# Optimization experiments

Measured on AMD Instinct MI355X. Metric: run time of the kernel, lower is better.

Reference implementation:

```python
import jax, jax.numpy as jnp
import numpy as np

H = 64        # HIDDEN_DIM
V = 64        # VOCAB_SIZE
INNER = 16    # INNER_DIM
LR = 0.01     # INFERENCE_LR
B = 256
L = 2048
EPS = 1e-5    # LayerNorm eps (torch default)


def setup_inputs() -> dict:
    key = jax.random.key(0)
    ks = jax.random.split(key, 8)

    def lin(k, fi, fo):
        return jax.random.normal(k, (fi, fo), jnp.float32) / np.sqrt(fi).astype(np.float32)

    return {
        "seq": jax.random.randint(ks[0], (B, L), 0, V),
        "embed": jax.random.normal(ks[1], (V, H), jnp.float32) * 0.02,
        "ff_w1": lin(ks[2], H, 2 * H), "ff_b1": jnp.zeros((2 * H,), jnp.float32),
        "ff_w2": lin(ks[3], 2 * H, H), "ff_b2": jnp.zeros((H,), jnp.float32),
        "ln_g": jnp.ones((H,), jnp.float32), "ln_b": jnp.zeros((H,), jnp.float32),
        "w1": lin(ks[4], H, INNER), "b1": jnp.zeros((INNER,), jnp.float32),
        "w2": lin(ks[5], INNER, H), "b2": jnp.zeros((H,), jnp.float32),
        "out_w": lin(ks[6], H, V), "out_b": jnp.zeros((V,), jnp.float32),
    }


def _mlp(p, x):
    W1, B1, W2, B2 = p
    return jnp.maximum(x @ W1 + B1, 0.0) @ W2 + B2


def reference(seq, embed, ff_w1, ff_b1, ff_w2, ff_b2, ln_g, ln_b,
              w1, b1, w2, b2, out_w, out_b):
    # Encoder: embed -> residual FFN -> LayerNorm
    e = embed[seq]                                        # [B,L,H]
    ff = jnp.maximum(e @ ff_w1 + ff_b1, 0.0) @ ff_w2 + ff_b2
    h = e + ff
    mu = h.mean(-1, keepdims=True)
    var = ((h - mu) ** 2).mean(-1, keepdims=True)
    hs = (h - mu) / jnp.sqrt(var + EPS) * ln_g + ln_b     # [B,L,H]
    hs = jax.lax.stop_gradient(hs)                        # all TTT inputs are .detach()ed in torch

    T = (L - 2) // 2                                      # len(range(0, L-3, 2))
    idx = jnp.arange(T) * 2
    k_seq = hs[:, idx]                                    # [B,T,H]
    v_seq = hs[:, idx + 1]                                # [B,T,H]

    # base params copied via load_state_dict -> no grad connection
    p0 = tuple(jax.lax.stop_gradient(p) for p in (w1, b1, w2, b2))

    def ttt(kseq, vseq, qlast):
        def step(p, kv):
            k, v = kv
            g = jax.grad(lambda pp: jnp.mean((_mlp(pp, k) - v) ** 2))(p)
            return jax.tree_util.tree_map(lambda a, ga: a - LR * ga, p, g), None
        pf, _ = jax.lax.scan(step, p0, (kseq, vseq))
        return _mlp(pf, qlast)                            # [H]

    ctx = jax.vmap(ttt)(k_seq, v_seq, hs[:, -1])          # [B,H]
    ctx = jax.lax.stop_gradient(ctx)                      # torch builds ctx under no_grad
    return ctx @ out_w + out_b                            # [B,V]
```

## Files before the change

kernel.cpp:

```cpp
#include <hip/hip_runtime.h>

#define TSTEPS 1023
#define GAMMA  (0.01f / 32.0f)
#define EPSV   1e-5f

#define WS_HS 0
#define WS_G  4096
#define WS_Z0 8192

typedef float v2f __attribute__((ext_vector_type(2)));
typedef unsigned int v2u __attribute__((ext_vector_type(2)));

template<int CTRL>
__device__ __forceinline__ float dppmov(float x) {
    return __int_as_float(__builtin_amdgcn_update_dpp(0, __float_as_int(x), CTRL, 0xF, 0xF, true));
}
__device__ __forceinline__ v2u swap16(float a, float b) {
    return __builtin_amdgcn_permlane16_swap(__float_as_uint(a), __float_as_uint(b), false, false);
}
__device__ __forceinline__ v2u swap32(float a, float b) {
    return __builtin_amdgcn_permlane32_swap(__float_as_uint(a), __float_as_uint(b), false, false);
}
__device__ __forceinline__ float rlane(float v, int sl) {
    return __int_as_float(__builtin_amdgcn_readlane(__float_as_int(v), sl));
}
#define U2F(x) __uint_as_float(x)

__global__ void hs_kernel(const float* __restrict__ embed,
                          const float* __restrict__ ffw1, const float* __restrict__ ffb1,
                          const float* __restrict__ ffw2, const float* __restrict__ ffb2,
                          const float* __restrict__ lng,  const float* __restrict__ lnb,
                          float* __restrict__ ws) {
    __shared__ float e[64];
    __shared__ float a1[128];
    int w = blockIdx.x;
    int tid = threadIdx.x;
    if (tid < 64) e[tid] = embed[w * 64 + tid];
    __syncthreads();
    float z1 = ffb1[tid];
    for (int x = 0; x < 64; ++x) z1 += e[x] * ffw1[x * 128 + tid];
    a1[tid] = fmaxf(z1, 0.0f);
    __syncthreads();
    if (tid < 64) {
        float f = ffb2[tid];
        for (int i = 0; i < 128; ++i) f += a1[i] * ffw2[i * 64 + tid];
        float hv = e[tid] + f;
        float s = hv;
#pragma unroll
        for (int m = 32; m >= 1; m >>= 1) s += __shfl_xor(s, m);
        float mu = s * (1.0f / 64.0f);
        float dv = hv - mu;
        float vs = dv * dv;
#pragma unroll
        for (int m = 32; m >= 1; m >>= 1) vs += __shfl_xor(vs, m);
        float rstd = 1.0f / sqrtf(vs * (1.0f / 64.0f) + EPSV);
        ws[WS_HS + w * 64 + tid] = dv * rstd * lng[tid] + lnb[tid];
    }
}

__global__ void gz_kernel(const float* __restrict__ w1, const float* __restrict__ b1,
                          float* __restrict__ ws) {
    __shared__ float row[64];
    int w = blockIdx.x, tid = threadIdx.x;
    row[tid] = ws[WS_HS + w * 64 + tid];
    __syncthreads();
    float g = 0.0f;
    for (int x = 0; x < 64; ++x) g += row[x] * ws[WS_HS + tid * 64 + x];
    ws[WS_G + w * 64 + tid] = GAMMA * g + GAMMA;
    if (tid < 16) {
        float z = b1[tid];
        for (int x = 0; x < 64; ++x) z += row[x] * w1[x * 16 + tid];
        ws[WS_Z0 + w * 16 + tid] = z;
    }
}

struct TTT4Smem {
    float hs[4096];
    float Gs[4096];
    int   sq[2048];
    float ybuf[2][4][64];
    float ctxp[4][64];
};

__device__ __forceinline__ void reduce4(const v2f* a2, const v2f* p2, v2f* dz2) {
    float q0 = p2[0].x + dppmov<0xB1>(p2[1].x);
    float q1 = p2[0].y + dppmov<0xB1>(p2[1].y);
    float rm0 = (a2[0].x > 0.0f) ? q0 : 0.0f;
    float rm1 = (a2[0].y > 0.0f) ? q1 : 0.0f;
    v2u f01 = swap16(rm0, rm1);
    float T = U2F(f01[0]) + U2F(f01[1]);
    v2u g01 = swap32(T, T);
    T = U2F(g01[0]) + U2F(g01[1]);
    T = T + dppmov<0x122>(T);
    T = T + dppmov<0x124>(T);
    T = T + dppmov<0x128>(T);
    v2u u01 = swap16(T, T);
    const float A0 = U2F(u01[0]);
    const float A1 = U2F(u01[1]);
    dz2[0] = {A0, A1};
    dz2[1] = {dppmov<0xB1>(A0), dppmov<0xB1>(A1)};
}

__launch_bounds__(256, 1)
__global__ void ttt_kernel(const int* __restrict__ seq,
                           const float* __restrict__ w2, const float* __restrict__ b2i,
                           const float* __restrict__ outw, const float* __restrict__ outb,
                           const float* __restrict__ ws, float* __restrict__ out) {
    __shared__ TTT4Smem sm;

    const int b    = blockIdx.x;
    const int tid  = threadIdx.x;
    const int wv   = tid >> 6;
    const int lane = tid & 63;
    const int b0   = lane & 1;
    const int X    = b0 << 1;
    const bool pb  = (b0 != 0);
    const bool wv0 = (wv == 0);

    {
        float4*       hv = (float4*)sm.hs;
        const float4* sv = (const float4*)(ws + WS_HS);
#pragma unroll
        for (int m = 0; m < 4; ++m) hv[m * 256 + tid] = sv[m * 256 + tid];
        float4*       gv = (float4*)sm.Gs;
        const float4* gs = (const float4*)(ws + WS_G);
#pragma unroll
        for (int m = 0; m < 4; ++m) gv[m * 256 + tid] = gs[m * 256 + tid];
        int4*       qv = (int4*)sm.sq;
        const int4* qs = (const int4*)(seq + b * 2048);
#pragma unroll
        for (int m = 0; m < 2; ++m) qv[m * 256 + tid] = qs[m * 256 + tid];
    }

    v2f Zv[2];
    {
        const float4 z0 = *(const float4*)(ws + WS_Z0 + lane * 16 + 4 * wv);
        Zv[0] = {z0.x, z0.y};
        Zv[1] = {z0.z, z0.w};
    }

    v2f W2p[2];
#pragma unroll
    for (int i = 0; i < 2; ++i) {
        v2f w;
        w.x = w2[(4 * wv + ((2 * i) ^ X)) * 64 + lane];
        w.y = w2[(4 * wv + ((2 * i + 1) ^ X)) * 64 + lane];
        W2p[i] = w;
    }
    float ybias = wv0 ? b2i[lane] : 0.0f;
    const float gma = wv0 ? GAMMA : 0.0f;
    __syncthreads();

    int tk = sm.sq[0];
    v2f z2[2];
    {
        const int stk = __builtin_amdgcn_readfirstlane(tk);
        const float e0 = rlane(Zv[0].x, stk);
        const float e1 = rlane(Zv[0].y, stk);
        const float e2 = rlane(Zv[1].x, stk);
        const float e3 = rlane(Zv[1].y, stk);
        z2[0] = { pb ? e2 : e0, pb ? e3 : e1 };
        z2[1] = { pb ? e0 : e2, pb ? e1 : e3 };
    }
    float vv = sm.hs[sm.sq[1] * 64 + lane];

    int2 pairT  = *(const int2*)(sm.sq + 2);
    int2 pairT1 = *(const int2*)(sm.sq + 4);

#pragma unroll 2
    for (int t = 0; t < TSTEPS - 1; ++t) {
        const int tkn = pairT.x;
        const int tvn = pairT.y;
        const int par = t & 1;

        const v2f zero2 = {0.0f, 0.0f};
        v2f a2[2];
        a2[0] = __builtin_elementwise_max(z2[0], zero2);
        a2[1] = __builtin_elementwise_max(z2[1], zero2);
        v2f accv = a2[0] * W2p[0] + a2[1] * W2p[1];
        const float ypart = ybias + accv.x + accv.y;

        sm.ybuf[par][wv][lane] = ypart;
        __syncthreads();
        const float y0 = sm.ybuf[par][0][lane];
        const float y1 = sm.ybuf[par][1][lane];
        const float y2 = sm.ybuf[par][2][lane];
        const float y3 = sm.ybuf[par][3][lane];

        const float vnext = sm.hs[tvn * 64 + lane];
        const float cr = sm.Gs[tk * 64 + lane];
        const int2 pairT2 = *(const int2*)(sm.sq + 2 * t + 6);
        const int stkn = __builtin_amdgcn_readfirstlane(tkn);
        const float e0 = rlane(Zv[0].x, stkn);
        const float e1 = rlane(Zv[0].y, stkn);
        const float e2 = rlane(Zv[1].x, stkn);
        const float e3 = rlane(Zv[1].y, stkn);
        const v2f E0 = { pb ? e2 : e0, pb ? e3 : e1 };
        const v2f E1 = { pb ? e0 : e2, pb ? e1 : e3 };
        const float cz = rlane(cr, stkn);

        const float d = ((y0 + y1) + (y2 + y3)) - vv;

        const v2f d2 = {d, d};
        v2f p2[2];
        p2[0] = W2p[0] * d2;
        p2[1] = W2p[1] * d2;
        const float sd = GAMMA * d;
        ybias -= gma * d;
        const v2f sd2 = {sd, sd};
        W2p[0] = W2p[0] - sd2 * a2[0];
        W2p[1] = W2p[1] - sd2 * a2[1];

        v2f dz2[2];
        reduce4(a2, p2, dz2);

        const v2f cz2 = {cz, cz};
        z2[0] = E0 - cz2 * dz2[0];
        z2[1] = E1 - cz2 * dz2[1];

        const v2f dzl0 = pb ? dz2[1] : dz2[0];
        const v2f dzl1 = pb ? dz2[0] : dz2[1];
        const v2f cr2 = {cr, cr};
        Zv[0] = Zv[0] - cr2 * dzl0;
        Zv[1] = Zv[1] - cr2 * dzl1;

        vv = vnext;
        tk = tkn;
        pairT = pairT1;
        pairT1 = pairT2;
    }

    {
        const int tkn = pairT.y;
        const v2f zero2 = {0.0f, 0.0f};
        v2f a2[2];
        a2[0] = __builtin_elementwise_max(z2[0], zero2);
        a2[1] = __builtin_elementwise_max(z2[1], zero2);
        v2f accv = a2[0] * W2p[0] + a2[1] * W2p[1];
        const float ypart = ybias + accv.x + accv.y;

        sm.ybuf[0][wv][lane] = ypart;
        __syncthreads();
        const float y0 = sm.ybuf[0][0][lane];
        const float y1 = sm.ybuf[0][1][lane];
        const float y2 = sm.ybuf[0][2][lane];
        const float y3 = sm.ybuf[0][3][lane];

        const float cr = sm.Gs[tk * 64 + lane];
        const int stkn = __builtin_amdgcn_readfirstlane(tkn);
        const float e0 = rlane(Zv[0].x, stkn);
        const float e1 = rlane(Zv[0].y, stkn);
        const float e2 = rlane(Zv[1].x, stkn);
        const float e3 = rlane(Zv[1].y, stkn);
        const v2f E0 = { pb ? e2 : e0, pb ? e3 : e1 };
        const v2f E1 = { pb ? e0 : e2, pb ? e1 : e3 };
        const float cz = rlane(cr, stkn);

        const float d = ((y0 + y1) + (y2 + y3)) - vv;

        const v2f d2 = {d, d};
        v2f p2[2];
        p2[0] = W2p[0] * d2;
        p2[1] = W2p[1] * d2;
        const float sd = GAMMA * d;
        ybias -= gma * d;
        const v2f sd2 = {sd, sd};
        W2p[0] = W2p[0] - sd2 * a2[0];
        W2p[1] = W2p[1] - sd2 * a2[1];

        v2f dz2[2];
        reduce4(a2, p2, dz2);

        const v2f cz2 = {cz, cz};
        z2[0] = E0 - cz2 * dz2[0];
        z2[1] = E1 - cz2 * dz2[1];
    }

    {
        const v2f zero2 = {0.0f, 0.0f};
        v2f acc = __builtin_elementwise_max(z2[0], zero2) * W2p[0]
                + __builtin_elementwise_max(z2[1], zero2) * W2p[1];
        sm.ctxp[wv][lane] = ybias + acc.x + acc.y;
    }
    __syncthreads();
    if (wv0) {
        float o = outb[lane];
        for (int hh = 0; hh < 64; ++hh)
            o += (sm.ctxp[0][hh] + sm.ctxp[1][hh] + sm.ctxp[2][hh] + sm.ctxp[3][hh])
                 * outw[hh * 64 + lane];
        out[b * 64 + lane] = o;
    }
}

extern "C" void kernel_launch(void* const* d_in, const int* in_sizes, int n_in,
                              void* d_out, int out_size, void* d_ws, size_t ws_size,
                              hipStream_t stream) {
    const int*   seq   = (const int*)d_in[0];
    const float* embed = (const float*)d_in[1];
    const float* ffw1  = (const float*)d_in[2];
    const float* ffb1  = (const float*)d_in[3];
    const float* ffw2  = (const float*)d_in[4];
    const float* ffb2  = (const float*)d_in[5];
    const float* lng   = (const float*)d_in[6];
    const float* lnb   = (const float*)d_in[7];
    const float* w1    = (const float*)d_in[8];
    const float* b1    = (const float*)d_in[9];
    const float* w2    = (const float*)d_in[10];
    const float* b2    = (const float*)d_in[11];
    const float* outw  = (const float*)d_in[12];
    const float* outb  = (const float*)d_in[13];
    float* ws  = (float*)d_ws;
    float* out = (float*)d_out;

    hipLaunchKernelGGL(hs_kernel, dim3(64), dim3(128), 0, stream,
                       embed, ffw1, ffb1, ffw2, ffb2, lng, lnb, ws);
    hipLaunchKernelGGL(gz_kernel, dim3(64), dim3(64), 0, stream, w1, b1, ws);
    hipLaunchKernelGGL(ttt_kernel, dim3(256), dim3(256), 0, stream,
                       seq, w2, b2, outw, outb, ws, out);
}
```

Before: 350.2 us.

## Compute backprop dz via maintained W2·W2ᵀ Gram matrix instead of per-step reduction

```diff
diff --git a/kernel.cpp b/kernel.cpp
--- a/kernel.cpp
+++ b/kernel.cpp
@@ -2,11 +2,13 @@
 
 #define TSTEPS 1023
 #define GAMMA  (0.01f / 32.0f)
+#define GAMMA2 (GAMMA * GAMMA)
 #define EPSV   1e-5f
 
 #define WS_HS 0
 #define WS_G  4096
 #define WS_Z0 8192
+#define WS_M  9216
 
 typedef float v2f __attribute__((ext_vector_type(2)));
 typedef unsigned int v2u __attribute__((ext_vector_type(2)));
@@ -74,20 +76,28 @@
     }
 }
 
+__global__ void m0_kernel(const float* __restrict__ w2, float* __restrict__ ws) {
+    int j = threadIdx.x >> 4, k = threadIdx.x & 15;
+    float acc = 0.0f;
+    for (int h = 0; h < 64; ++h) acc += w2[j * 64 + h] * w2[k * 64 + h];
+    ws[WS_M + threadIdx.x] = acc;
+}
+
 struct TTT4Smem {
     float hs[4096];
     float Gs[4096];
     int   sq[2048];
     float ybuf[2][4][64];
+    float abuf[2][16];
+    float cbuf[2][16];
+    float dbuf[2];
     float ctxp[4][64];
 };
 
-__device__ __forceinline__ void reduce4(const v2f* a2, const v2f* p2, v2f* dz2) {
+__device__ __forceinline__ void reduceS(const v2f* p2, v2f* out) {
     float q0 = p2[0].x + dppmov<0xB1>(p2[1].x);
     float q1 = p2[0].y + dppmov<0xB1>(p2[1].y);
-    float rm0 = (a2[0].x > 0.0f) ? q0 : 0.0f;
-    float rm1 = (a2[0].y > 0.0f) ? q1 : 0.0f;
-    v2u f01 = swap16(rm0, rm1);
+    v2u f01 = swap16(q0, q1);
     float T = U2F(f01[0]) + U2F(f01[1]);
     v2u g01 = swap32(T, T);
     T = U2F(g01[0]) + U2F(g01[1]);
@@ -97,8 +107,14 @@
     v2u u01 = swap16(T, T);
     const float A0 = U2F(u01[0]);
     const float A1 = U2F(u01[1]);
-    dz2[0] = {A0, A1};
-    dz2[1] = {dppmov<0xB1>(A0), dppmov<0xB1>(A1)};
+    out[0] = {A0, A1};
+    out[1] = {dppmov<0xB1>(A0), dppmov<0xB1>(A1)};
+}
+
+__device__ __forceinline__ float pubsel(const v2f* x2, int lane) {
+    float odd  = (lane & 2) ? x2[0].y : x2[1].y;
+    float even = (lane & 2) ? x2[1].x : x2[0].x;
+    return (lane & 1) ? odd : even;
 }
 
 __launch_bounds__(256, 1)
@@ -147,7 +163,9 @@
         w.y = w2[(4 * wv + ((2 * i + 1) ^ X)) * 64 + lane];
         W2p[i] = w;
     }
-    float ybias = wv0 ? b2i[lane] : 0.0f;
+    float Mreg = ws[WS_M + (4 * wv + (lane >> 4)) * 16 + (lane & 15)];
+    const float bful = b2i[lane];
+    float ybias = wv0 ? bful : 0.0f;
     const float gma = wv0 ? GAMMA : 0.0f;
     __syncthreads();
 
@@ -164,8 +182,24 @@
     }
     float vv = sm.hs[sm.sq[1] * 64 + lane];
 
+    v2f m2[2], s2[2];
+    {
+        const v2f bb = {bful, bful};
+        v2f p0[2] = { W2p[0] * bb, W2p[1] * bb };
+        reduceS(p0, m2);
+        const v2f vs0 = {vv, vv};
+        v2f p1[2] = { W2p[0] * vs0, W2p[1] * vs0 };
+        reduceS(p1, s2);
+    }
+
+    float avp = 0.0f, ajp = 0.0f, ddv = 0.0f, db2pub = 0.0f;
+    v2f cs_prev[2] = {{0.0f, 0.0f}, {0.0f, 0.0f}};
+    v2f as_prev[2] = {{0.0f, 0.0f}, {0.0f, 0.0f}};
+
     int2 pairT  = *(const int2*)(sm.sq + 2);
     int2 pairT1 = *(const int2*)(sm.sq + 4);
+
+    const v2f zero2 = {0.0f, 0.0f};
 
 #pragma unroll 2
     for (int t = 0; t < TSTEPS - 1; ++t) {
@@ -173,7 +207,6 @@
         const int tvn = pairT.y;
         const int par = t & 1;
 
-        const v2f zero2 = {0.0f, 0.0f};
         v2f a2[2];
         a2[0] = __builtin_elementwise_max(z2[0], zero2);
         a2[1] = __builtin_elementwise_max(z2[1], zero2);
@@ -181,15 +214,55 @@
         const float ypart = ybias + accv.x + accv.y;
 
         sm.ybuf[par][wv][lane] = ypart;
+        if (lane < 4) {
+            sm.abuf[par][4 * wv + lane] = pubsel(a2, lane);
+            sm.cbuf[par][4 * wv + lane] = pubsel(cs_prev, lane);
+        }
+        if (wv0 && lane == 0) sm.dbuf[par] = db2pub;
         __syncthreads();
+
         const float y0 = sm.ybuf[par][0][lane];
         const float y1 = sm.ybuf[par][1][lane];
         const float y2 = sm.ybuf[par][2][lane];
         const float y3 = sm.ybuf[par][3][lane];
-
+        const float av   = sm.abuf[par][lane & 15];
+        const float ajn  = sm.abuf[par][4 * wv + (lane >> 4)];
+        const float ck   = sm.cbuf[par][lane & 15];
+        const float cjn  = sm.cbuf[par][4 * wv + (lane >> 4)];
+        const float db2s = sm.dbuf[par];
         const float vnext = sm.hs[tvn * 64 + lane];
         const float cr = sm.Gs[tk * 64 + lane];
         const int2 pairT2 = *(const int2*)(sm.sq + 2 * t + 6);
+
+        const float t1 = ddv * GAMMA2;
+        const float Aj = t1 * ajp - GAMMA * cjn;
+        Mreg = Mreg + avp * Aj - (GAMMA * ajp) * ck;
+
+        const float S = t1 - GAMMA * db2s;
+        const v2f Sv = {S, S};
+        const v2f Gm = {GAMMA, GAMMA};
+        m2[0] = m2[0] - Gm * cs_prev[0] + Sv * as_prev[0];
+        m2[1] = m2[1] - Gm * cs_prev[1] + Sv * as_prev[1];
+
+        float ur = Mreg * av;
+        ur += dppmov<0x121>(ur);
+        ur += dppmov<0x122>(ur);
+        ur += dppmov<0x124>(ur);
+        ur += dppmov<0x128>(ur);
+        const float uj0 = rlane(ur, 0);
+        const float uj1 = rlane(ur, 16);
+        const float uj2 = rlane(ur, 32);
+        const float uj3 = rlane(ur, 48);
+        const v2f Ulo = {uj0, uj1};
+        const v2f Uhi = {uj2, uj3};
+
+        v2f c2[2];
+        c2[0] = (pb ? Uhi : Ulo) + m2[0] - s2[0];
+        c2[1] = (pb ? Ulo : Uhi) + m2[1] - s2[1];
+        v2f dz2[2];
+        dz2[0] = { a2[0].x > 0.0f ? c2[0].x : 0.0f, a2[0].y > 0.0f ? c2[0].y : 0.0f };
+        dz2[1] = { a2[1].x > 0.0f ? c2[1].x : 0.0f, a2[1].y > 0.0f ? c2[1].y : 0.0f };
+
         const int stkn = __builtin_amdgcn_readfirstlane(tkn);
         const float e0 = rlane(Zv[0].x, stkn);
         const float e1 = rlane(Zv[0].y, stkn);
@@ -199,24 +272,35 @@
         const v2f E1 = { pb ? e0 : e2, pb ? e1 : e3 };
         const float cz = rlane(cr, stkn);
 
+        const v2f cz2 = {cz, cz};
+        z2[0] = E0 - cz2 * dz2[0];
+        z2[1] = E1 - cz2 * dz2[1];
+
         const float d = ((y0 + y1) + (y2 + y3)) - vv;
-
-        const v2f d2 = {d, d};
-        v2f p2[2];
-        p2[0] = W2p[0] * d2;
-        p2[1] = W2p[1] * d2;
+        const float Qv = d * ybias;
         const float sd = GAMMA * d;
         ybias -= gma * d;
         const v2f sd2 = {sd, sd};
         W2p[0] = W2p[0] - sd2 * a2[0];
         W2p[1] = W2p[1] - sd2 * a2[1];
 
-        v2f dz2[2];
-        reduce4(a2, p2, dz2);
-
-        const v2f cz2 = {cz, cz};
-        z2[0] = E0 - cz2 * dz2[0];
-        z2[1] = E1 - cz2 * dz2[1];
+        float P = d * d, Q = Qv;
+        P += dppmov<0xB1>(P);  Q += dppmov<0xB1>(Q);
+        P += dppmov<0x4E>(P);  Q += dppmov<0x4E>(Q);
+        P += dppmov<0x124>(P); Q += dppmov<0x124>(Q);
+        P += dppmov<0x128>(P); Q += dppmov<0x128>(Q);
+        v2u pq = swap16(P, Q);
+        float T2 = U2F(pq[0]) + U2F(pq[1]);
+        v2u pq2 = swap32(T2, T2);
+        T2 = U2F(pq2[0]) + U2F(pq2[1]);
+        const float ddn   = rlane(T2, 0);
+        const float db2n  = rlane(T2, 16);
+
+        {
+            const v2f vs2 = {vnext, vnext};
+            v2f ps[2] = { W2p[0] * vs2, W2p[1] * vs2 };
+            reduceS(ps, s2);
+        }
 
         const v2f dzl0 = pb ? dz2[1] : dz2[0];
         const v2f dzl1 = pb ? dz2[0] : dz2[1];
@@ -224,6 +308,11 @@
         Zv[0] = Zv[0] - cr2 * dzl0;
         Zv[1] = Zv[1] - cr2 * dzl1;
 
+        avp = av; ajp = ajn;
+        cs_prev[0] = c2[0]; cs_prev[1] = c2[1];
+        as_prev[0] = a2[0]; as_prev[1] = a2[1];
+        ddv = ddn; db2pub = db2n;
+
         vv = vnext;
         tk = tkn;
         pairT = pairT1;
@@ -232,7 +321,6 @@
 
     {
         const int tkn = pairT.y;
-        const v2f zero2 = {0.0f, 0.0f};
         v2f a2[2];
         a2[0] = __builtin_elementwise_max(z2[0], zero2);
         a2[1] = __builtin_elementwise_max(z2[1], zero2);
@@ -240,13 +328,53 @@
         const float ypart = ybias + accv.x + accv.y;
 
         sm.ybuf[0][wv][lane] = ypart;
+        if (lane < 4) {
+            sm.abuf[0][4 * wv + lane] = pubsel(a2, lane);
+            sm.cbuf[0][4 * wv + lane] = pubsel(cs_prev, lane);
+        }
+        if (wv0 && lane == 0) sm.dbuf[0] = db2pub;
         __syncthreads();
+
         const float y0 = sm.ybuf[0][0][lane];
         const float y1 = sm.ybuf[0][1][lane];
         const float y2 = sm.ybuf[0][2][lane];
         const float y3 = sm.ybuf[0][3][lane];
-
+        const float av   = sm.abuf[0][lane & 15];
+        const float ajn  = sm.abuf[0][4 * wv + (lane >> 4)];
+        const float ck   = sm.cbuf[0][lane & 15];
+        const float cjn  = sm.cbuf[0][4 * wv + (lane >> 4)];
+        const float db2s = sm.dbuf[0];
         const float cr = sm.Gs[tk * 64 + lane];
+
+        const float t1 = ddv * GAMMA2;
+        const float Aj = t1 * ajp - GAMMA * cjn;
+        Mreg = Mreg + avp * Aj - (GAMMA * ajp) * ck;
+
+        const float S = t1 - GAMMA * db2s;
+        const v2f Sv = {S, S};
+        const v2f Gm = {GAMMA, GAMMA};
+        m2[0] = m2[0] - Gm * cs_prev[0] + Sv * as_prev[0];
+        m2[1] = m2[1] - Gm * cs_prev[1] + Sv * as_prev[1];
+
+        float ur = Mreg * av;
+        ur += dppmov<0x121>(ur);
+        ur += dppmov<0x122>(ur);
+        ur += dppmov<0x124>(ur);
+        ur += dppmov<0x128>(ur);
+        const float uj0 = rlane(ur, 0);
+        const float uj1 = rlane(ur, 16);
+        const float uj2 = rlane(ur, 32);
+        const float uj3 = rlane(ur, 48);
+        const v2f Ulo = {uj0, uj1};
+        const v2f Uhi = {uj2, uj3};
+
+        v2f c2[2];
+        c2[0] = (pb ? Uhi : Ulo) + m2[0] - s2[0];
+        c2[1] = (pb ? Ulo : Uhi) + m2[1] - s2[1];
+        v2f dz2[2];
+        dz2[0] = { a2[0].x > 0.0f ? c2[0].x : 0.0f, a2[0].y > 0.0f ? c2[0].y : 0.0f };
+        dz2[1] = { a2[1].x > 0.0f ? c2[1].x : 0.0f, a2[1].y > 0.0f ? c2[1].y : 0.0f };
+
         const int stkn = __builtin_amdgcn_readfirstlane(tkn);
         const float e0 = rlane(Zv[0].x, stkn);
         const float e1 = rlane(Zv[0].y, stkn);
@@ -256,28 +384,19 @@
         const v2f E1 = { pb ? e0 : e2, pb ? e1 : e3 };
         const float cz = rlane(cr, stkn);
 
+        const v2f cz2 = {cz, cz};
+        z2[0] = E0 - cz2 * dz2[0];
+        z2[1] = E1 - cz2 * dz2[1];
+
         const float d = ((y0 + y1) + (y2 + y3)) - vv;
-
-        const v2f d2 = {d, d};
-        v2f p2[2];
-        p2[0] = W2p[0] * d2;
-        p2[1] = W2p[1] * d2;
         const float sd = GAMMA * d;
         ybias -= gma * d;
         const v2f sd2 = {sd, sd};
         W2p[0] = W2p[0] - sd2 * a2[0];
         W2p[1] = W2p[1] - sd2 * a2[1];
-
-        v2f dz2[2];
-        reduce4(a2, p2, dz2);
-
-        const v2f cz2 = {cz, cz};
-        z2[0] = E0 - cz2 * dz2[0];
-        z2[1] = E1 - cz2 * dz2[1];
-    }
-
-    {
-        const v2f zero2 = {0.0f, 0.0f};
+    }
+
+    {
         v2f acc = __builtin_elementwise_max(z2[0], zero2) * W2p[0]
                 + __builtin_elementwise_max(z2[1], zero2) * W2p[1];
         sm.ctxp[wv][lane] = ybias + acc.x + acc.y;
@@ -315,6 +434,7 @@
     hipLaunchKernelGGL(hs_kernel, dim3(64), dim3(128), 0, stream,
                        embed, ffw1, ffb1, ffw2, ffb2, lng, lnb, ws);
     hipLaunchKernelGGL(gz_kernel, dim3(64), dim3(64), 0, stream, w1, b1, ws);
+    hipLaunchKernelGGL(m0_kernel, dim3(1), dim3(256), 0, stream, w2, ws);
     hipLaunchKernelGGL(ttt_kernel, dim3(256), dim3(256), 0, stream,
                        seq, w2, b2, outw, outb, ws, out);
 }
```

After: 556.6 us. 59.0% more time.

## Fuse encoder and Gram precompute kernels into the TTT kernel

Applied to the files above, without the earlier changes.

```diff
diff --git a/kernel.cpp b/kernel.cpp
--- a/kernel.cpp
+++ b/kernel.cpp
@@ -4,11 +4,8 @@
 #define GAMMA  (0.01f / 32.0f)
 #define EPSV   1e-5f
 
-#define WS_HS 0
-#define WS_G  4096
-#define WS_Z0 8192
-
 typedef float v2f __attribute__((ext_vector_type(2)));
+typedef float v4f __attribute__((ext_vector_type(4)));
 typedef unsigned int v2u __attribute__((ext_vector_type(2)));
 
 template<int CTRL>
@@ -26,60 +23,15 @@
 }
 #define U2F(x) __uint_as_float(x)
 
-__global__ void hs_kernel(const float* __restrict__ embed,
-                          const float* __restrict__ ffw1, const float* __restrict__ ffb1,
-                          const float* __restrict__ ffw2, const float* __restrict__ ffb2,
-                          const float* __restrict__ lng,  const float* __restrict__ lnb,
-                          float* __restrict__ ws) {
-    __shared__ float e[64];
-    __shared__ float a1[128];
-    int w = blockIdx.x;
-    int tid = threadIdx.x;
-    if (tid < 64) e[tid] = embed[w * 64 + tid];
-    __syncthreads();
-    float z1 = ffb1[tid];
-    for (int x = 0; x < 64; ++x) z1 += e[x] * ffw1[x * 128 + tid];
-    a1[tid] = fmaxf(z1, 0.0f);
-    __syncthreads();
-    if (tid < 64) {
-        float f = ffb2[tid];
-        for (int i = 0; i < 128; ++i) f += a1[i] * ffw2[i * 64 + tid];
-        float hv = e[tid] + f;
-        float s = hv;
-#pragma unroll
-        for (int m = 32; m >= 1; m >>= 1) s += __shfl_xor(s, m);
-        float mu = s * (1.0f / 64.0f);
-        float dv = hv - mu;
-        float vs = dv * dv;
-#pragma unroll
-        for (int m = 32; m >= 1; m >>= 1) vs += __shfl_xor(vs, m);
-        float rstd = 1.0f / sqrtf(vs * (1.0f / 64.0f) + EPSV);
-        ws[WS_HS + w * 64 + tid] = dv * rstd * lng[tid] + lnb[tid];
-    }
-}
-
-__global__ void gz_kernel(const float* __restrict__ w1, const float* __restrict__ b1,
-                          float* __restrict__ ws) {
-    __shared__ float row[64];
-    int w = blockIdx.x, tid = threadIdx.x;
-    row[tid] = ws[WS_HS + w * 64 + tid];
-    __syncthreads();
-    float g = 0.0f;
-    for (int x = 0; x < 64; ++x) g += row[x] * ws[WS_HS + tid * 64 + x];
-    ws[WS_G + w * 64 + tid] = GAMMA * g + GAMMA;
-    if (tid < 16) {
-        float z = b1[tid];
-        for (int x = 0; x < 64; ++x) z += row[x] * w1[x * 16 + tid];
-        ws[WS_Z0 + w * 16 + tid] = z;
-    }
-}
-
-struct TTT4Smem {
+struct TTTSmem {
     float hs[4096];
     float Gs[4096];
     int   sq[2048];
     float ybuf[2][4][64];
     float ctxp[4][64];
+    float zbuf[1024];
+    float a1T[8192];
+    float scratch[8192];
 };
 
 __device__ __forceinline__ void reduce4(const v2f* a2, const v2f* p2, v2f* dz2) {
@@ -103,10 +55,15 @@
 
 __launch_bounds__(256, 1)
 __global__ void ttt_kernel(const int* __restrict__ seq,
-                           const float* __restrict__ w2, const float* __restrict__ b2i,
+                           const float* __restrict__ embed,
+                           const float* __restrict__ ffw1, const float* __restrict__ ffb1,
+                           const float* __restrict__ ffw2, const float* __restrict__ ffb2,
+                           const float* __restrict__ lng,  const float* __restrict__ lnb,
+                           const float* __restrict__ w1,   const float* __restrict__ b1,
+                           const float* __restrict__ w2,   const float* __restrict__ b2i,
                            const float* __restrict__ outw, const float* __restrict__ outb,
-                           const float* __restrict__ ws, float* __restrict__ out) {
-    __shared__ TTT4Smem sm;
+                           float* __restrict__ out) {
+    __shared__ TTTSmem sm;
 
     const int b    = blockIdx.x;
     const int tid  = threadIdx.x;
@@ -118,23 +75,142 @@
     const bool wv0 = (wv == 0);
 
     {
-        float4*       hv = (float4*)sm.hs;
-        const float4* sv = (const float4*)(ws + WS_HS);
-#pragma unroll
-        for (int m = 0; m < 4; ++m) hv[m * 256 + tid] = sv[m * 256 + tid];
-        float4*       gv = (float4*)sm.Gs;
-        const float4* gs = (const float4*)(ws + WS_G);
-#pragma unroll
-        for (int m = 0; m < 4; ++m) gv[m * 256 + tid] = gs[m * 256 + tid];
         int4*       qv = (int4*)sm.sq;
         const int4* qs = (const int4*)(seq + b * 2048);
-#pragma unroll
-        for (int m = 0; m < 2; ++m) qv[m * 256 + tid] = qs[m * 256 + tid];
-    }
+        qv[tid]       = qs[tid];
+        qv[256 + tid] = qs[256 + tid];
+        const v4f* e4 = (const v4f*)embed;
+#pragma unroll
+        for (int p = 0; p < 4; ++p) {
+            int i4 = p * 256 + tid;
+            v4f v = e4[i4];
+            ((v4f*)sm.hs)[i4] = v;
+            int w = i4 >> 4, h0 = (i4 & 15) << 2;
+            sm.Gs[(h0 + 0) * 64 + w] = v.x;
+            sm.Gs[(h0 + 1) * 64 + w] = v.y;
+            sm.Gs[(h0 + 2) * 64 + w] = v.z;
+            sm.Gs[(h0 + 3) * 64 + w] = v.w;
+        }
+        const v4f* f14 = (const v4f*)ffw1;
+        v4f* s4 = (v4f*)sm.scratch;
+#pragma unroll
+        for (int p = 0; p < 8; ++p) s4[p * 256 + tid] = f14[p * 256 + tid];
+    }
+    __syncthreads();
+
+    {
+        const int g = tid >> 5, iq = tid & 31;
+        v4f bb = *(const v4f*)(ffb1 + 4 * iq);
+        v4f acc[8];
+#pragma unroll
+        for (int ww = 0; ww < 8; ++ww) acc[ww] = bb;
+        for (int x = 0; x < 64; ++x) {
+            v4f f  = *(const v4f*)(sm.scratch + x * 128 + 4 * iq);
+            v4f ea = *(const v4f*)(sm.Gs + x * 64 + 8 * g);
+            v4f eb = *(const v4f*)(sm.Gs + x * 64 + 8 * g + 4);
+            acc[0] += ea.x * f; acc[1] += ea.y * f;
+            acc[2] += ea.z * f; acc[3] += ea.w * f;
+            acc[4] += eb.x * f; acc[5] += eb.y * f;
+            acc[6] += eb.z * f; acc[7] += eb.w * f;
+        }
+#pragma unroll
+        for (int ww = 0; ww < 8; ++ww) {
+            int w = 8 * g + ww;
+#pragma unroll
+            for (int ii = 0; ii < 4; ++ii)
+                sm.a1T[(4 * iq + ii) * 64 + w] = fmaxf(acc[ww][ii], 0.0f);
+        }
+    }
+    __syncthreads();
+
+    {
+        const v4f* f24 = (const v4f*)ffw2;
+        v4f* s4 = (v4f*)sm.scratch;
+#pragma unroll
+        for (int p = 0; p < 8; ++p) s4[p * 256 + tid] = f24[p * 256 + tid];
+    }
+    __syncthreads();
+
+    {
+        const int g2 = tid >> 4, hq = tid & 15;
+        v4f bb = *(const v4f*)(ffb2 + 4 * hq);
+        v4f acc[4];
+#pragma unroll
+        for (int ww = 0; ww < 4; ++ww) acc[ww] = bb;
+        for (int i = 0; i < 128; ++i) {
+            v4f f = *(const v4f*)(sm.scratch + i * 64 + 4 * hq);
+            v4f a = *(const v4f*)(sm.a1T + i * 64 + 4 * g2);
+            acc[0] += a.x * f; acc[1] += a.y * f;
+            acc[2] += a.z * f; acc[3] += a.w * f;
+        }
+        v4f g4 = *(const v4f*)(lng + 4 * hq);
+        v4f l4 = *(const v4f*)(lnb + 4 * hq);
+#pragma unroll
+        for (int ww = 0; ww < 4; ++ww) {
+            int w = 4 * g2 + ww;
+            v4f ev = *(const v4f*)(sm.hs + w * 64 + 4 * hq);
+            v4f hv = ev + acc[ww];
+            float ps = (hv.x + hv.y) + (hv.z + hv.w);
+            ps += dppmov<0x121>(ps);
+            ps += dppmov<0x122>(ps);
+            ps += dppmov<0x124>(ps);
+            ps += dppmov<0x128>(ps);
+            float mu = ps * (1.0f / 64.0f);
+            v4f dv = hv - mu;
+            float pv = (dv.x * dv.x + dv.y * dv.y) + (dv.z * dv.z + dv.w * dv.w);
+            pv += dppmov<0x121>(pv);
+            pv += dppmov<0x122>(pv);
+            pv += dppmov<0x124>(pv);
+            pv += dppmov<0x128>(pv);
+            float rstd = 1.0f / sqrtf(pv * (1.0f / 64.0f) + EPSV);
+            v4f r = dv * rstd * g4 + l4;
+            *(v4f*)(sm.hs + w * 64 + 4 * hq) = r;
+        }
+    }
+    __syncthreads();
+
+#pragma unroll
+    for (int p = 0; p < 16; ++p) {
+        int idx = p * 256 + tid;
+        sm.scratch[(idx & 63) * 64 + (idx >> 6)] = sm.hs[idx];
+    }
+    __syncthreads();
+
+    {
+        const int g3 = tid >> 4, tq = tid & 15;
+        v4f acc[4] = {{0,0,0,0},{0,0,0,0},{0,0,0,0},{0,0,0,0}};
+        for (int xb = 0; xb < 16; ++xb) {
+            v4f hw0 = *(const v4f*)(sm.hs + (4 * g3 + 0) * 64 + 4 * xb);
+            v4f hw1 = *(const v4f*)(sm.hs + (4 * g3 + 1) * 64 + 4 * xb);
+            v4f hw2 = *(const v4f*)(sm.hs + (4 * g3 + 2) * 64 + 4 * xb);
+            v4f hw3 = *(const v4f*)(sm.hs + (4 * g3 + 3) * 64 + 4 * xb);
+#pragma unroll
+            for (int xx = 0; xx < 4; ++xx) {
+                v4f hT = *(const v4f*)(sm.scratch + (4 * xb + xx) * 64 + 4 * tq);
+                acc[0] += hw0[xx] * hT;
+                acc[1] += hw1[xx] * hT;
+                acc[2] += hw2[xx] * hT;
+                acc[3] += hw3[xx] * hT;
+            }
+        }
+#pragma unroll
+        for (int ww = 0; ww < 4; ++ww) {
+            v4f r = acc[ww] * GAMMA + GAMMA;
+            *(v4f*)(sm.Gs + (4 * g3 + ww) * 64 + 4 * tq) = r;
+        }
+        v4f accz = *(const v4f*)(b1 + 4 * wv);
+        for (int x = 0; x < 64; ++x) {
+            float hx = sm.scratch[x * 64 + lane];
+            v4f w4 = *(const v4f*)(w1 + x * 16 + 4 * wv);
+            accz += hx * w4;
+        }
+        *(v4f*)(sm.zbuf + lane * 16 + 4 * wv) = accz;
+    }
+    __syncthreads();
 
     v2f Zv[2];
     {
-        const float4 z0 = *(const float4*)(ws + WS_Z0 + lane * 16 + 4 * wv);
+        v4f z0 = *(const v4f*)(sm.zbuf + lane * 16 + 4 * wv);
         Zv[0] = {z0.x, z0.y};
         Zv[1] = {z0.z, z0.w};
     }
@@ -149,7 +225,6 @@
     }
     float ybias = wv0 ? b2i[lane] : 0.0f;
     const float gma = wv0 ? GAMMA : 0.0f;
-    __syncthreads();
 
     int tk = sm.sq[0];
     v2f z2[2];
@@ -309,12 +384,9 @@
     const float* b2    = (const float*)d_in[11];
     const float* outw  = (const float*)d_in[12];
     const float* outb  = (const float*)d_in[13];
-    float* ws  = (float*)d_ws;
     float* out = (float*)d_out;
 
-    hipLaunchKernelGGL(hs_kernel, dim3(64), dim3(128), 0, stream,
-                       embed, ffw1, ffb1, ffw2, ffb2, lng, lnb, ws);
-    hipLaunchKernelGGL(gz_kernel, dim3(64), dim3(64), 0, stream, w1, b1, ws);
     hipLaunchKernelGGL(ttt_kernel, dim3(256), dim3(256), 0, stream,
-                       seq, w2, b2, outw, outb, ws, out);
-}
+                       seq, embed, ffw1, ffb1, ffw2, ffb2, lng, lnb,
+                       w1, b1, w2, b2, outw, outb, out);
+}
```

Measured after the change: 389.1 us. 11.1% more time.
